# Performance work log

Hardware: AMD Instinct MI355X
Metric: run time of the kernel (lower is better)

Reference implementation:

```python
import jax, jax.numpy as jnp
import numpy as np

WIN = 3  # window_size (stride fixed to 1, matching module defaults)


def setup_inputs() -> dict:
    key = jax.random.key(0)
    ks = jax.random.split(key, 5)
    B, D, L = 4, 768, 4096
    s = 1.0 / np.sqrt(D)  # PyTorch nn.RNN init: U(-1/sqrt(hidden), 1/sqrt(hidden))
    return {
        "x": jax.random.normal(ks[0], (B, D, L), dtype=jnp.float32),
        "W_ih": jax.random.uniform(ks[1], (D, D), jnp.float32, -s, s),
        "W_hh": jax.random.uniform(ks[2], (D, D), jnp.float32, -s, s),
        "b_ih": jax.random.uniform(ks[3], (D,), jnp.float32, -s, s),
        "b_hh": jax.random.uniform(ks[4], (D,), jnp.float32, -s, s),
        "gamma": jnp.ones((L,), jnp.float32),  # LayerNorm over length axis
        "beta": jnp.zeros((L,), jnp.float32),
    }


def reference(x, W_ih, W_hh, b_ih, b_hh, gamma, beta):
    # x: [B, D, L]. For each position i, run a 1-layer ReLU RNN (h0=0) over the
    B, D, L = x.shape
    xt = jnp.transpose(x, (2, 0, 1))  # [L, B, D] (seq-first, like the torch code)
    xp = jnp.concatenate([jnp.zeros((WIN - 1, B, D), x.dtype), xt], axis=0)  # left-pad
    idx = jnp.arange(L)[:, None] + jnp.arange(WIN)[None, :]
    win = xp[idx]
    valid = (jnp.arange(L)[:, None] - (WIN - 1) + jnp.arange(WIN)[None, :]) >= 0

    def step(h, tw):
        x_t, m = tw  # x_t: [L, B, D], m: [L]
        hn = jax.nn.relu(x_t @ W_ih.T + b_ih + h @ W_hh.T + b_hh)
        # invalid (pre-window) steps keep h unchanged (stays 0) => exact short-window semantics
        return jnp.where(m[:, None, None], hn, h), None

    h0 = jnp.zeros((L, B, D), x.dtype)
    h, _ = jax.lax.scan(step, h0, (jnp.transpose(win, (1, 0, 2, 3)), valid.T))
    enc = jnp.transpose(h, (1, 2, 0))  # [B, D, L]

    # residual + LayerNorm with normalized_shape=(L,), eps=1e-12, affine (gamma=1, beta=0 at init)
    z = enc + x
    mean = jnp.mean(z, axis=-1, keepdims=True)
    var = jnp.var(z, axis=-1, keepdims=True)
    return (z - mean) / jnp.sqrt(var + 1e-12) * gamma + beta
```

## Files before the change

### kernel.cpp

```cpp
#include <hip/hip_runtime.h>

typedef unsigned short u16;
typedef __bf16 bf16x8 __attribute__((ext_vector_type(8)));
typedef float f32x4 __attribute__((ext_vector_type(4)));

#define Bq 4
#define Dq 768
#define Lq 4096
#define Mq (Lq * Bq)

__device__ __forceinline__ u16 f2bf(float f) {
    unsigned int u = __builtin_bit_cast(unsigned int, f);
    u += 0x7fffu + ((u >> 16) & 1u);
    return (u16)(u >> 16);
}

__device__ __forceinline__ void async16(const void* g, void* l) {
    __builtin_amdgcn_global_load_lds(
        (const __attribute__((address_space(1))) unsigned int*)(unsigned long long)g,
        (__attribute__((address_space(3))) unsigned int*)(unsigned int)(unsigned long long)l,
        16, 0, 0);
}

__global__ __launch_bounds__(256) void prep_kernel(
    const float* __restrict__ Wih, const float* __restrict__ Whh,
    u16* __restrict__ Wihb, u16* __restrict__ Whhb,
    u16* __restrict__ Vpad, u16* __restrict__ Gpad) {
    int i = blockIdx.x * 256 + threadIdx.x;
    if (i < Dq * Dq) {
        Wihb[i] = f2bf(Wih[i]);
        Whhb[i] = f2bf(Whh[i]);
    }
    if (i < Bq * Dq) { Vpad[i] = 0; Gpad[i] = 0; }
}

__global__ __launch_bounds__(256) void transpose_kernel(
    const float* __restrict__ x, u16* __restrict__ Xt) {
    __shared__ u16 tile[64][66];
    int b = blockIdx.z, d0 = blockIdx.y * 64, l0 = blockIdx.x * 64;
    int tx = threadIdx.x & 63, ty = threadIdx.x >> 6;
    const float* xp = x + ((size_t)b * Dq + d0) * Lq + l0;
#pragma unroll
    for (int i = 0; i < 16; ++i) {
        int r = i * 4 + ty;
        tile[r][tx] = f2bf(xp[(size_t)r * Lq + tx]);
    }
    __syncthreads();
    u16* xt = Xt + ((size_t)l0 * Bq + b) * Dq + d0;
#pragma unroll
    for (int i = 0; i < 16; ++i) {
        int c = i * 4 + ty;
        xt[(size_t)c * Bq * Dq + tx] = tile[tx][c];
    }
}

template <int MODE>
__global__ __launch_bounds__(256) void gemm_kernel(
    const u16* __restrict__ A, const u16* __restrict__ W,
    float* __restrict__ U, u16* __restrict__ OutBf,
    float* __restrict__ Eout,
    const float* __restrict__ bih, const float* __restrict__ bhh) {
    extern __shared__ __align__(16) char smem[];
    u16* As = (u16*)smem;
    u16* Bs = (u16*)(smem + 8192);
    float* ep = (float*)(smem + 16384);

    int tid = threadIdx.x;
    int wave = tid >> 6, lane = tid & 63;
    int wr = wave >> 1, wc = wave & 1;
    int m0 = blockIdx.y * 128, n0 = blockIdx.x * 128;
    int lr = lane & 15, lq = lane >> 4;

    int srow = wave * 32 + (lane >> 2);
    int scol = (lane & 3) * 8;
    const u16* ga = A + (size_t)(m0 + srow) * Dq + scol;
    const u16* gb = W + (size_t)(n0 + srow) * Dq + scol;
    u16* laA0 = As + (wave * 32) * 32;
    u16* laA1 = As + (wave * 32 + 16) * 32;
    u16* laB0 = Bs + (wave * 32) * 32;
    u16* laB1 = Bs + (wave * 32 + 16) * 32;

    f32x4 acc[4][4];
#pragma unroll
    for (int i = 0; i < 4; ++i)
#pragma unroll
        for (int j = 0; j < 4; ++j) acc[i][j] = f32x4{0.f, 0.f, 0.f, 0.f};

    for (int k0 = 0; k0 < Dq; k0 += 32) {
        async16(ga, laA0);
        async16(ga + 16 * Dq, laA1);
        async16(gb, laB0);
        async16(gb + 16 * Dq, laB1);
        ga += 32; gb += 32;
        __syncthreads();

        bf16x8 af[4], bfr[4];
#pragma unroll
        for (int mt = 0; mt < 4; ++mt)
            af[mt] = *(const bf16x8*)(As + (wr * 64 + mt * 16 + lr) * 32 + lq * 8);
#pragma unroll
        for (int nt = 0; nt < 4; ++nt)
            bfr[nt] = *(const bf16x8*)(Bs + (wc * 64 + nt * 16 + lr) * 32 + lq * 8);
#pragma unroll
        for (int mt = 0; mt < 4; ++mt)
#pragma unroll
            for (int nt = 0; nt < 4; ++nt)
                acc[mt][nt] = __builtin_amdgcn_mfma_f32_16x16x32_bf16(
                    af[mt], bfr[nt], acc[mt][nt], 0, 0, 0);
        __syncthreads();
    }

    if constexpr (MODE == 1) {
#pragma unroll
        for (int nt = 0; nt < 4; ++nt) {
            int gn = n0 + wc * 64 + nt * 16 + lr;
            float bi = bih[gn], bh = bhh[gn];
#pragma unroll
            for (int mt = 0; mt < 4; ++mt) {
                int gm = m0 + wr * 64 + mt * 16 + lq * 4;
                f32x4 v = acc[mt][nt];
#pragma unroll
                for (int r = 0; r < 4; ++r) {
                    float u = v[r] + bi;
                    U[(size_t)(gm + r) * Dq + gn] = u;
                    OutBf[(size_t)(gm + r + Bq) * Dq + gn] = f2bf(fmaxf(u + bh, 0.f));
                }
            }
        }
    } else if constexpr (MODE == 2) {
#pragma unroll
        for (int nt = 0; nt < 4; ++nt) {
            int gn = n0 + wc * 64 + nt * 16 + lr;
            float bh = bhh[gn];
#pragma unroll
            for (int mt = 0; mt < 4; ++mt) {
                int gm = m0 + wr * 64 + mt * 16 + lq * 4;
                f32x4 v = acc[mt][nt];
#pragma unroll
                for (int r = 0; r < 4; ++r) {
                    float g = fmaxf(U[(size_t)(gm + r) * Dq + gn] + bh + v[r], 0.f);
                    OutBf[(size_t)(gm + r + Bq) * Dq + gn] = f2bf(g);
                }
            }
        }
    } else {
        float* epw = ep + wave * (64 * 17);
        int l0w = (m0 >> 2) + wr * 16;
#pragma unroll
        for (int nt = 0; nt < 4; ++nt) {
            int gn = n0 + wc * 64 + nt * 16 + lr;
            float bh = bhh[gn];
#pragma unroll
            for (int mt = 0; mt < 4; ++mt) {
                int lmb = mt * 16 + lq * 4;
                int gm = m0 + wr * 64 + lmb;
                f32x4 v = acc[mt][nt];
#pragma unroll
                for (int r = 0; r < 4; ++r) {
                    float e = fmaxf(U[(size_t)(gm + r) * Dq + gn] + bh + v[r], 0.f);
                    epw[(lmb + r) * 17 + lr] = e;
                }
            }
            __syncthreads();
            int bb = lane >> 4, cc = lane & 15;
            int gnc = n0 + wc * 64 + nt * 16 + cc;
            float vals[16];
#pragma unroll
            for (int ll = 0; ll < 16; ++ll)
                vals[ll] = epw[(ll * 4 + bb) * 17 + cc];
            float* dst = Eout + (size_t)bb * (Dq * Lq) + (size_t)gnc * Lq + l0w;
#pragma unroll
            for (int s = 0; s < 4; ++s) {
                f32x4 w4 = {vals[s * 4], vals[s * 4 + 1], vals[s * 4 + 2], vals[s * 4 + 3]};
                *(f32x4*)(dst + s * 4) = w4;
            }
            __syncthreads();
        }
    }
}

__global__ __launch_bounds__(256) void ln_kernel(
    const float* __restrict__ E, const float* __restrict__ x,
    const float* __restrict__ gamma, const float* __restrict__ beta,
    float* __restrict__ out) {
    __shared__ float red[2][4];
    size_t row = blockIdx.x;
    const float* e = E + row * Lq;
    const float* xr = x + row * Lq;
    float* o = out + row * Lq;
    int t = threadIdx.x;
    float z[16];
    float s = 0.f, sq = 0.f;
#pragma unroll
    for (int i = 0; i < 4; ++i) {
        int idx = (i * 256 + t) * 4;
        f32x4 ev = *(const f32x4*)(e + idx);
        f32x4 xv = *(const f32x4*)(xr + idx);
#pragma unroll
        for (int j = 0; j < 4; ++j) {
            float zz = ev[j] + xv[j];
            z[i * 4 + j] = zz;
            s += zz;
            sq += zz * zz;
        }
    }
#pragma unroll
    for (int off = 32; off > 0; off >>= 1) {
        s += __shfl_down(s, off);
        sq += __shfl_down(sq, off);
    }
    int wave = t >> 6, lane = t & 63;
    if (lane == 0) { red[0][wave] = s; red[1][wave] = sq; }
    __syncthreads();
    s = red[0][0] + red[0][1] + red[0][2] + red[0][3];
    sq = red[1][0] + red[1][1] + red[1][2] + red[1][3];
    float mean = s * (1.f / Lq);
    float var = sq * (1.f / Lq) - mean * mean;
    float rstd = rsqrtf(var + 1e-12f);
#pragma unroll
    for (int i = 0; i < 4; ++i) {
        int idx = (i * 256 + t) * 4;
        f32x4 gv = *(const f32x4*)(gamma + idx);
        f32x4 bv = *(const f32x4*)(beta + idx);
        f32x4 ov;
#pragma unroll
        for (int j = 0; j < 4; ++j)
            ov[j] = (z[i * 4 + j] - mean) * rstd * gv[j] + bv[j];
        *(f32x4*)(o + idx) = ov;
    }
}

extern "C" void kernel_launch(void* const* d_in, const int* in_sizes, int n_in,
                              void* d_out, int out_size, void* d_ws, size_t ws_size,
                              hipStream_t stream) {
    const float* x     = (const float*)d_in[0];
    const float* Wih   = (const float*)d_in[1];
    const float* Whh   = (const float*)d_in[2];
    const float* bih   = (const float*)d_in[3];
    const float* bhh   = (const float*)d_in[4];
    const float* gamma = (const float*)d_in[5];
    const float* beta  = (const float*)d_in[6];
    float* out = (float*)d_out;

    char* ws = (char*)d_ws;
    u16* Xt    = (u16*)ws;              ws += (size_t)Mq * Dq * 2;
    u16* Wihb  = (u16*)ws;              ws += (size_t)Dq * Dq * 2;
    u16* Whhb  = (u16*)ws;              ws += (size_t)Dq * Dq * 2;
    float* U   = (float*)ws;            ws += (size_t)Mq * Dq * 4;
    u16* Vpad  = (u16*)ws;              ws += (size_t)(Mq + Bq) * Dq * 2;
    u16* Gpad  = (u16*)ws;              ws += (size_t)(Mq + Bq) * Dq * 2;
    float* Eout = (float*)ws;           ws += (size_t)Mq * Dq * 4;

    prep_kernel<<<dim3((Dq * Dq + 255) / 256), 256, 0, stream>>>(
        Wih, Whh, Wihb, Whhb, Vpad, Gpad);
    transpose_kernel<<<dim3(Lq / 64, Dq / 64, Bq), 256, 0, stream>>>(x, Xt);

    dim3 ggrid(Dq / 128, Mq / 128);
    gemm_kernel<1><<<ggrid, 256, 16384, stream>>>(Xt,   Wihb, U, Vpad, nullptr, bih, bhh);
    gemm_kernel<2><<<ggrid, 256, 16384, stream>>>(Vpad, Whhb, U, Gpad, nullptr, bih, bhh);
    gemm_kernel<3><<<ggrid, 256, 33792, stream>>>(Gpad, Whhb, U, nullptr, Eout, bih, bhh);

    ln_kernel<<<dim3(Bq * Dq), 256, 0, stream>>>(Eout, x, gamma, beta, out);
}
```

Before: 287.2 us.

## Recompute input projection in-GEMM instead of storing fp32 U; bf16 encoder output

Drops the fp32 U intermediate. Steps 2 and 3 now run a two-segment K loop that recomputes X·Wih^T alongside h·Whh^T, which cuts large fp32 global reads and writes at the cost of doubling the MFMA work in those GEMMs. The encoder output is stored as bf16 and read as bf16 by the LayerNorm kernel, halving that traffic but adding rounding error. It also widens the K step to 64 per barrier and swaps the grid axes so M runs along blockIdx.x.

```diff
diff --git a/kernel.cpp b/kernel.cpp
--- a/kernel.cpp
+++ b/kernel.cpp
@@ -3,6 +3,7 @@
 typedef unsigned short u16;
 typedef __bf16 bf16x8 __attribute__((ext_vector_type(8)));
 typedef float f32x4 __attribute__((ext_vector_type(4)));
+typedef unsigned short u16x8 __attribute__((ext_vector_type(8)));
 
 #define Bq 4
 #define Dq 768
@@ -13,6 +14,10 @@
     unsigned int u = __builtin_bit_cast(unsigned int, f);
     u += 0x7fffu + ((u >> 16) & 1u);
     return (u16)(u >> 16);
+}
+
+__device__ __forceinline__ float bf2f(u16 h) {
+    return __builtin_bit_cast(float, (unsigned int)h << 16);
 }
 
 __device__ __forceinline__ void async16(const void* g, void* l) {
@@ -54,31 +59,34 @@
     }
 }
 
-template <int MODE>
+template <int NSEG, int MODE>
 __global__ __launch_bounds__(256) void gemm_kernel(
-    const u16* __restrict__ A, const u16* __restrict__ W,
-    float* __restrict__ U, u16* __restrict__ OutBf,
-    float* __restrict__ Eout,
+    const u16* __restrict__ A0, const u16* __restrict__ W0,
+    const u16* __restrict__ A1, const u16* __restrict__ W1,
+    u16* __restrict__ Out,
     const float* __restrict__ bih, const float* __restrict__ bhh) {
-    extern __shared__ __align__(16) char smem[];
-    u16* As = (u16*)smem;
-    u16* Bs = (u16*)(smem + 8192);
-    float* ep = (float*)(smem + 16384);
+    __shared__ __align__(16) char smem[32768];
+    u16* As0 = (u16*)smem;
+    u16* As1 = As0 + 4096;
+    u16* Bs0 = As0 + 8192;
+    u16* Bs1 = As0 + 12288;
 
     int tid = threadIdx.x;
     int wave = tid >> 6, lane = tid & 63;
     int wr = wave >> 1, wc = wave & 1;
-    int m0 = blockIdx.y * 128, n0 = blockIdx.x * 128;
+    int m0 = blockIdx.x * 128, n0 = blockIdx.y * 128;
     int lr = lane & 15, lq = lane >> 4;
 
     int srow = wave * 32 + (lane >> 2);
     int scol = (lane & 3) * 8;
-    const u16* ga = A + (size_t)(m0 + srow) * Dq + scol;
-    const u16* gb = W + (size_t)(n0 + srow) * Dq + scol;
-    u16* laA0 = As + (wave * 32) * 32;
-    u16* laA1 = As + (wave * 32 + 16) * 32;
-    u16* laB0 = Bs + (wave * 32) * 32;
-    u16* laB1 = Bs + (wave * 32 + 16) * 32;
+    u16* lA0a = As0 + (wave * 32) * 32;
+    u16* lA0b = As0 + (wave * 32 + 16) * 32;
+    u16* lA1a = As1 + (wave * 32) * 32;
+    u16* lA1b = As1 + (wave * 32 + 16) * 32;
+    u16* lB0a = Bs0 + (wave * 32) * 32;
+    u16* lB0b = Bs0 + (wave * 32 + 16) * 32;
+    u16* lB1a = Bs1 + (wave * 32) * 32;
+    u16* lB1b = Bs1 + (wave * 32 + 16) * 32;
 
     f32x4 acc[4][4];
 #pragma unroll
@@ -86,80 +94,76 @@
 #pragma unroll
         for (int j = 0; j < 4; ++j) acc[i][j] = f32x4{0.f, 0.f, 0.f, 0.f};
 
-    for (int k0 = 0; k0 < Dq; k0 += 32) {
-        async16(ga, laA0);
-        async16(ga + 16 * Dq, laA1);
-        async16(gb, laB0);
-        async16(gb + 16 * Dq, laB1);
-        ga += 32; gb += 32;
-        __syncthreads();
-
-        bf16x8 af[4], bfr[4];
-#pragma unroll
-        for (int mt = 0; mt < 4; ++mt)
-            af[mt] = *(const bf16x8*)(As + (wr * 64 + mt * 16 + lr) * 32 + lq * 8);
-#pragma unroll
-        for (int nt = 0; nt < 4; ++nt)
-            bfr[nt] = *(const bf16x8*)(Bs + (wc * 64 + nt * 16 + lr) * 32 + lq * 8);
-#pragma unroll
-        for (int mt = 0; mt < 4; ++mt)
-#pragma unroll
-            for (int nt = 0; nt < 4; ++nt)
-                acc[mt][nt] = __builtin_amdgcn_mfma_f32_16x16x32_bf16(
-                    af[mt], bfr[nt], acc[mt][nt], 0, 0, 0);
-        __syncthreads();
-    }
-
-    if constexpr (MODE == 1) {
+#pragma unroll
+    for (int seg = 0; seg < NSEG; ++seg) {
+        const u16* Ab = (seg == 0) ? A0 : A1;
+        const u16* Wb = (seg == 0) ? W0 : W1;
+        const u16* ga = Ab + (size_t)(m0 + srow) * Dq + scol;
+        const u16* gb = Wb + (size_t)(n0 + srow) * Dq + scol;
+
+        for (int k0 = 0; k0 < Dq; k0 += 64) {
+            async16(ga,               lA0a);
+            async16(ga + 16 * Dq,     lA0b);
+            async16(ga + 32,          lA1a);
+            async16(ga + 16 * Dq + 32, lA1b);
+            async16(gb,               lB0a);
+            async16(gb + 16 * Dq,     lB0b);
+            async16(gb + 32,          lB1a);
+            async16(gb + 16 * Dq + 32, lB1b);
+            ga += 64; gb += 64;
+            __syncthreads();
+
+#pragma unroll
+            for (int s = 0; s < 2; ++s) {
+                const u16* Asub = s ? As1 : As0;
+                const u16* Bsub = s ? Bs1 : Bs0;
+                bf16x8 af[4], bfr[4];
+#pragma unroll
+                for (int mt = 0; mt < 4; ++mt)
+                    af[mt] = *(const bf16x8*)(Asub + (wr * 64 + mt * 16 + lr) * 32 + lq * 8);
+#pragma unroll
+                for (int nt = 0; nt < 4; ++nt)
+                    bfr[nt] = *(const bf16x8*)(Bsub + (wc * 64 + nt * 16 + lr) * 32 + lq * 8);
+#pragma unroll
+                for (int mt = 0; mt < 4; ++mt)
+#pragma unroll
+                    for (int nt = 0; nt < 4; ++nt)
+                        acc[mt][nt] = __builtin_amdgcn_mfma_f32_16x16x32_bf16(
+                            af[mt], bfr[nt], acc[mt][nt], 0, 0, 0);
+            }
+            __syncthreads();
+        }
+    }
+
+    if constexpr (MODE == 0) {
 #pragma unroll
         for (int nt = 0; nt < 4; ++nt) {
             int gn = n0 + wc * 64 + nt * 16 + lr;
-            float bi = bih[gn], bh = bhh[gn];
+            float bsum = bih[gn] + bhh[gn];
 #pragma unroll
             for (int mt = 0; mt < 4; ++mt) {
                 int gm = m0 + wr * 64 + mt * 16 + lq * 4;
                 f32x4 v = acc[mt][nt];
 #pragma unroll
-                for (int r = 0; r < 4; ++r) {
-                    float u = v[r] + bi;
-                    U[(size_t)(gm + r) * Dq + gn] = u;
-                    OutBf[(size_t)(gm + r + Bq) * Dq + gn] = f2bf(fmaxf(u + bh, 0.f));
-                }
+                for (int r = 0; r < 4; ++r)
+                    Out[(size_t)(gm + r + Bq) * Dq + gn] = f2bf(fmaxf(v[r] + bsum, 0.f));
             }
         }
-    } else if constexpr (MODE == 2) {
+    } else {
+        float* ep = (float*)smem;
+        float* epw = ep + wave * (64 * 17);
+        int l0w = (m0 >> 2) + wr * 16;
 #pragma unroll
         for (int nt = 0; nt < 4; ++nt) {
             int gn = n0 + wc * 64 + nt * 16 + lr;
-            float bh = bhh[gn];
-#pragma unroll
-            for (int mt = 0; mt < 4; ++mt) {
-                int gm = m0 + wr * 64 + mt * 16 + lq * 4;
-                f32x4 v = acc[mt][nt];
-#pragma unroll
-                for (int r = 0; r < 4; ++r) {
-                    float g = fmaxf(U[(size_t)(gm + r) * Dq + gn] + bh + v[r], 0.f);
-                    OutBf[(size_t)(gm + r + Bq) * Dq + gn] = f2bf(g);
-                }
-            }
-        }
-    } else {
-        float* epw = ep + wave * (64 * 17);
-        int l0w = (m0 >> 2) + wr * 16;
-#pragma unroll
-        for (int nt = 0; nt < 4; ++nt) {
-            int gn = n0 + wc * 64 + nt * 16 + lr;
-            float bh = bhh[gn];
+            float bsum = bih[gn] + bhh[gn];
 #pragma unroll
             for (int mt = 0; mt < 4; ++mt) {
                 int lmb = mt * 16 + lq * 4;
-                int gm = m0 + wr * 64 + lmb;
                 f32x4 v = acc[mt][nt];
 #pragma unroll
-                for (int r = 0; r < 4; ++r) {
-                    float e = fmaxf(U[(size_t)(gm + r) * Dq + gn] + bh + v[r], 0.f);
-                    epw[(lmb + r) * 17 + lr] = e;
-                }
+                for (int r = 0; r < 4; ++r)
+                    epw[(lmb + r) * 17 + lr] = fmaxf(v[r] + bsum, 0.f);
             }
             __syncthreads();
             int bb = lane >> 4, cc = lane & 15;
@@ -168,40 +172,43 @@
 #pragma unroll
             for (int ll = 0; ll < 16; ++ll)
                 vals[ll] = epw[(ll * 4 + bb) * 17 + cc];
-            float* dst = Eout + (size_t)bb * (Dq * Lq) + (size_t)gnc * Lq + l0w;
-#pragma unroll
-            for (int s = 0; s < 4; ++s) {
-                f32x4 w4 = {vals[s * 4], vals[s * 4 + 1], vals[s * 4 + 2], vals[s * 4 + 3]};
-                *(f32x4*)(dst + s * 4) = w4;
-            }
+            u16* dst = Out + (size_t)bb * (Dq * Lq) + (size_t)gnc * Lq + l0w;
+            u16x8 h0, h1;
+#pragma unroll
+            for (int j = 0; j < 8; ++j) { h0[j] = f2bf(vals[j]); h1[j] = f2bf(vals[8 + j]); }
+            *(u16x8*)dst = h0;
+            *(u16x8*)(dst + 8) = h1;
             __syncthreads();
         }
     }
 }
 
 __global__ __launch_bounds__(256) void ln_kernel(
-    const float* __restrict__ E, const float* __restrict__ x,
+    const u16* __restrict__ E, const float* __restrict__ x,
     const float* __restrict__ gamma, const float* __restrict__ beta,
     float* __restrict__ out) {
     __shared__ float red[2][4];
     size_t row = blockIdx.x;
-    const float* e = E + row * Lq;
+    const u16x8* e8 = (const u16x8*)(E + row * Lq);
     const float* xr = x + row * Lq;
     float* o = out + row * Lq;
     int t = threadIdx.x;
     float z[16];
     float s = 0.f, sq = 0.f;
 #pragma unroll
-    for (int i = 0; i < 4; ++i) {
-        int idx = (i * 256 + t) * 4;
-        f32x4 ev = *(const f32x4*)(e + idx);
-        f32x4 xv = *(const f32x4*)(xr + idx);
+    for (int i = 0; i < 2; ++i) {
+        int c = i * 256 + t;
+        u16x8 ev = e8[c];
+        f32x4 xv0 = *(const f32x4*)(xr + c * 8);
+        f32x4 xv1 = *(const f32x4*)(xr + c * 8 + 4);
 #pragma unroll
         for (int j = 0; j < 4; ++j) {
-            float zz = ev[j] + xv[j];
-            z[i * 4 + j] = zz;
-            s += zz;
-            sq += zz * zz;
+            float z0 = bf2f(ev[j]) + xv0[j];
+            float z1 = bf2f(ev[4 + j]) + xv1[j];
+            z[i * 8 + j] = z0;
+            z[i * 8 + 4 + j] = z1;
+            s += z0 + z1;
+            sq += z0 * z0 + z1 * z1;
         }
     }
 #pragma unroll
@@ -218,15 +225,19 @@
     float var = sq * (1.f / Lq) - mean * mean;
     float rstd = rsqrtf(var + 1e-12f);
 #pragma unroll
-    for (int i = 0; i < 4; ++i) {
-        int idx = (i * 256 + t) * 4;
-        f32x4 gv = *(const f32x4*)(gamma + idx);
-        f32x4 bv = *(const f32x4*)(beta + idx);
-        f32x4 ov;
-#pragma unroll
-        for (int j = 0; j < 4; ++j)
-            ov[j] = (z[i * 4 + j] - mean) * rstd * gv[j] + bv[j];
-        *(f32x4*)(o + idx) = ov;
+    for (int i = 0; i < 2; ++i) {
+        int c = i * 256 + t;
+#pragma unroll
+        for (int h = 0; h < 2; ++h) {
+            int idx = c * 8 + h * 4;
+            f32x4 gv = *(const f32x4*)(gamma + idx);
+            f32x4 bv = *(const f32x4*)(beta + idx);
+            f32x4 ov;
+#pragma unroll
+            for (int j = 0; j < 4; ++j)
+                ov[j] = (z[i * 8 + h * 4 + j] - mean) * rstd * gv[j] + bv[j];
+            *(f32x4*)(o + idx) = ov;
+        }
     }
 }
 
@@ -243,22 +254,21 @@
     float* out = (float*)d_out;
 
     char* ws = (char*)d_ws;
-    u16* Xt    = (u16*)ws;              ws += (size_t)Mq * Dq * 2;
-    u16* Wihb  = (u16*)ws;              ws += (size_t)Dq * Dq * 2;
-    u16* Whhb  = (u16*)ws;              ws += (size_t)Dq * Dq * 2;
-    float* U   = (float*)ws;            ws += (size_t)Mq * Dq * 4;
-    u16* Vpad  = (u16*)ws;              ws += (size_t)(Mq + Bq) * Dq * 2;
-    u16* Gpad  = (u16*)ws;              ws += (size_t)(Mq + Bq) * Dq * 2;
-    float* Eout = (float*)ws;           ws += (size_t)Mq * Dq * 4;
+    u16* Xt    = (u16*)ws;   ws += (size_t)Mq * Dq * 2;
+    u16* Wihb  = (u16*)ws;   ws += (size_t)Dq * Dq * 2;
+    u16* Whhb  = (u16*)ws;   ws += (size_t)Dq * Dq * 2;
+    u16* Vpad  = (u16*)ws;   ws += (size_t)(Mq + Bq) * Dq * 2;
+    u16* Gpad  = (u16*)ws;   ws += (size_t)(Mq + Bq) * Dq * 2;
+    u16* Eout  = (u16*)ws;   ws += (size_t)Mq * Dq * 2;
 
     prep_kernel<<<dim3((Dq * Dq + 255) / 256), 256, 0, stream>>>(
         Wih, Whh, Wihb, Whhb, Vpad, Gpad);
     transpose_kernel<<<dim3(Lq / 64, Dq / 64, Bq), 256, 0, stream>>>(x, Xt);
 
-    dim3 ggrid(Dq / 128, Mq / 128);
-    gemm_kernel<1><<<ggrid, 256, 16384, stream>>>(Xt,   Wihb, U, Vpad, nullptr, bih, bhh);
-    gemm_kernel<2><<<ggrid, 256, 16384, stream>>>(Vpad, Whhb, U, Gpad, nullptr, bih, bhh);
-    gemm_kernel<3><<<ggrid, 256, 33792, stream>>>(Gpad, Whhb, U, nullptr, Eout, bih, bhh);
+    dim3 ggrid(Mq / 128, Dq / 128);
+    gemm_kernel<1, 0><<<ggrid, 256, 0, stream>>>(Xt, Wihb, nullptr, nullptr, Vpad, bih, bhh);
+    gemm_kernel<2, 0><<<ggrid, 256, 0, stream>>>(Xt, Wihb, Vpad, Whhb, Gpad, bih, bhh);
+    gemm_kernel<2, 1><<<ggrid, 256, 0, stream>>>(Xt, Wihb, Gpad, Whhb, Eout, bih, bhh);
 
     ln_kernel<<<dim3(Bq * Dq), 256, 0, stream>>>(Eout, x, gamma, beta, out);
 }
```

New measurement: 275.1 us. 1.04x faster.
